# Performance work log

Hardware: AMD Instinct MI355X
Metric: run time of the kernel (lower is better)

The kernel has to match this reference:

```python
import jax, jax.numpy as jnp
import numpy as np

N_NODES = 50000
NEG_SLOPE = 0.2  # PyG GATConv default leaky_relu slope


def gat_conv(x, src, dst, W, a_src, a_dst, b, heads, out_ch, concat):
    """PyG-style GATConv. src/dst: [E] edge endpoints (messages flow src->dst)."""
    n = N_NODES
    h = (x @ W).reshape(n, heads, out_ch)            # [N, H, C]
    # per-node attention logits, gathered per edge
    s_src = (h * a_src).sum(-1)                       # [N, H]
    s_dst = (h * a_dst).sum(-1)                       # [N, H]
    e = jax.nn.leaky_relu(s_src[src] + s_dst[dst], NEG_SLOPE)  # [E, H]
    # segment softmax over incoming edges of each dst node
    e_max = jax.ops.segment_max(e, dst, num_segments=n)        # [N, H]
    ex = jnp.exp(e - e_max[dst])                                # [E, H]
    denom = jax.ops.segment_sum(ex, dst, num_segments=n)       # [N, H]
    alpha = ex / denom[dst]                                     # [E, H]
    # scatter-add weighted messages
    out = jax.ops.segment_sum(h[src] * alpha[:, :, None], dst, num_segments=n)  # [N, H, C]
    if concat:
        out = out.reshape(n, heads * out_ch)
    else:
        out = out.mean(axis=1)
    return out + b


def setup_inputs() -> dict:
    key = jax.random.key(0)
    ks = jax.random.split(key, 16)
    n, e = N_NODES, 400000
    in_ch, hidden, out_ch = 3, 64, 32
    x = jax.random.normal(ks[0], (n, in_ch), dtype=jnp.float32)
    edge_index = jax.random.randint(ks[1], (2, e), 0, n, dtype=jnp.int32)

    def glorot(k, shape):
        fan = sum(shape)
        return jax.random.uniform(k, shape, jnp.float32, -1.0, 1.0) * jnp.sqrt(6.0 / fan)

    # layer 1: in=3 -> hidden=64, heads=4, concat
    W1 = glorot(ks[2], (in_ch, 4 * hidden))
    a_src1 = glorot(ks[3], (4, hidden))
    a_dst1 = glorot(ks[4], (4, hidden))
    b1 = jnp.zeros((4 * hidden,), jnp.float32)
    # layer 2: 256 -> 64, heads=4, concat
    W2 = glorot(ks[5], (4 * hidden, 4 * hidden))
    a_src2 = glorot(ks[6], (4, hidden))
    a_dst2 = glorot(ks[7], (4, hidden))
    b2 = jnp.zeros((4 * hidden,), jnp.float32)
    # layer 3: 256 -> 32, heads=1, mean (concat=False)
    W3 = glorot(ks[8], (4 * hidden, out_ch))
    a_src3 = glorot(ks[9], (1, out_ch))
    a_dst3 = glorot(ks[10], (1, out_ch))
    b3 = jnp.zeros((out_ch,), jnp.float32)
    return dict(x=x, edge_index=edge_index,
                W1=W1, a_src1=a_src1, a_dst1=a_dst1, b1=b1,
                W2=W2, a_src2=a_src2, a_dst2=a_dst2, b2=b2,
                W3=W3, a_src3=a_src3, a_dst3=a_dst3, b3=b3)


def reference(x, edge_index,
              W1, a_src1, a_dst1, b1,
              W2, a_src2, a_dst2, b2,
              W3, a_src3, a_dst3, b3):
    n = N_NODES
    loops = jnp.arange(n, dtype=edge_index.dtype)
    src = jnp.concatenate([edge_index[0], loops])  # PyG adds self-loops by default
    dst = jnp.concatenate([edge_index[1], loops])
    h = gat_conv(x, src, dst, W1, a_src1, a_dst1, b1, heads=4, out_ch=64, concat=True)
    h = jax.nn.relu(h)  # dropout is identity in eval mode
    h = gat_conv(h, src, dst, W2, a_src2, a_dst2, b2, heads=4, out_ch=64, concat=True)
    h = jax.nn.relu(h)
    out = gat_conv(h, src, dst, W3, a_src3, a_dst3, b3, heads=1, out_ch=32, concat=False)
    return out
```

## Files before the change

kernel.cpp:

```cpp
#include <hip/hip_runtime.h>
#include <math.h>


#define NEG_SLOPE 0.2f
#define CAP 40

typedef unsigned short u16;
typedef short bf16x8 __attribute__((ext_vector_type(8)));
typedef float floatx4 __attribute__((ext_vector_type(4)));

__device__ __forceinline__ float b2f(u16 u) {
    return __uint_as_float(((unsigned int)u) << 16);
}
__device__ __forceinline__ u16 f2b(float f) {
    unsigned int u = __float_as_uint(f);
    unsigned int r = (u + 0x7fffu + ((u >> 16) & 1u)) >> 16;
    return (u16)r;
}
__device__ __forceinline__ void load16(const u16* g, u16* l) {
    __builtin_amdgcn_global_load_lds(
        (const __attribute__((address_space(1))) void*)g,
        (__attribute__((address_space(3))) void*)l, 16, 0, 0);
}


__device__ __forceinline__ void pack_dev(const float* __restrict__ W,
                                         u16* __restrict__ Bhi,
                                         u16* __restrict__ Blo, int N, int idx) {
    int CT = N / 16;
    int lane = idx & 63;
    int ctkb = idx >> 6;
    int ct = ctkb % CT;
    int kb = ctkb / CT;
    int col = ct * 16 + (lane & 15);
    int k0 = kb * 32 + (lane >> 4) * 8;
#pragma unroll
    for (int j = 0; j < 8; ++j) {
        float w = W[(size_t)(k0 + j) * N + col];
        u16 hi = f2b(w);
        Bhi[(size_t)idx * 8 + j] = hi;
        Blo[(size_t)idx * 8 + j] = f2b(w - b2f(hi));
    }
}


__global__ __launch_bounds__(256) void fill_prep(
    const int* __restrict__ ei,
    const float* __restrict__ W1, const float* __restrict__ as1,
    const float* __restrict__ ad1,
    const float* __restrict__ W2, const float* __restrict__ W3,
    u16* __restrict__ B2h, u16* __restrict__ B2l,
    u16* __restrict__ B3h, u16* __restrict__ B3l,
    float* __restrict__ vsd, int* __restrict__ cursor,
    int* __restrict__ csr, int n, int E) {
    const int tid = threadIdx.x;
    const int tg = blockIdx.x * 256 + tid;
    const int NTH = gridDim.x * 256;
    const int Etot = E + n;
    const int lane = tid & 63;

    if (tg < 8192) {
        pack_dev(W2, B2h, B2l, 256, tg);
    } else if (tg < 9216) {
        pack_dev(W3, B3h, B3l, 32, tg - 8192);
    } else if (tg < 9472) {
        int j = tg - 9216;
        float a_s = as1[j], a_d = ad1[j];
#pragma unroll
        for (int k = 0; k < 3; ++k) {
            float w = W1[k * 256 + j];
            float ps = w * a_s, pd = w * a_d;
#pragma unroll
            for (int o = 32; o > 0; o >>= 1) {
                ps += __shfl_xor(ps, o);
                pd += __shfl_xor(pd, o);
            }
            if (lane == 0) {
                vsd[(j >> 6) * 3 + k] = ps;
                vsd[12 + (j >> 6) * 3 + k] = pd;
            }
        }
    }
    for (int e = tg; e < Etot; e += NTH) {
        int src, dst;
        if (e < E) { src = ei[e]; dst = ei[E + e]; }
        else       { src = e - E; dst = e - E; }
        int old = atomicAdd(&cursor[dst], 1);
        if (old < CAP) csr[dst * CAP + old] = src;
    }
}


__global__ __launch_bounds__(256) void gat_aggregate_l1(const float* __restrict__ x,
                                                        const float* __restrict__ vsd,
                                                        const int* __restrict__ cur,
                                                        const int* __restrict__ csr,
                                                        const float* __restrict__ W1,
                                                        const float* __restrict__ bias,
                                                        u16* __restrict__ outHi,
                                                        u16* __restrict__ outLo, int n) {
    int node = blockIdx.x * 4 + (threadIdx.x >> 6);
    int lane = threadIdx.x & 63;
    if (node >= n) return;
    const int hB = lane & 3;
    const int eL = lane >> 2;
    const int hA = lane >> 4;
    int beg = node * CAP;
    int end = beg + min(cur[node], CAP);

    float vs0 = vsd[hB * 3 + 0], vs1 = vsd[hB * 3 + 1], vs2 = vsd[hB * 3 + 2];
    float vd0 = vsd[12 + hB * 3 + 0], vd1 = vsd[12 + hB * 3 + 1], vd2 = vsd[12 + hB * 3 + 2];
    float xd0 = x[node * 3 + 0], xd1 = x[node * 3 + 1], xd2 = x[node * 3 + 2];
    float sd = fmaf(xd0, vd0, fmaf(xd1, vd1, xd2 * vd2));

    float m = -INFINITY, l = 0.f;
    float ax = 0.f, ay = 0.f, az = 0.f;

    for (int base = beg; base < end; base += 16) {
        int j = base + eL;
        bool valid = (j < end);
        int sj = valid ? csr[j] : 0;
        float x0 = x[sj * 3 + 0];
        float x1 = x[sj * 3 + 1];
        float x2 = x[sj * 3 + 2];
        float logit = -INFINITY;
        if (valid) {
            float xv = fmaf(x0, vs0, fmaf(x1, vs1, x2 * vs2)) + sd;
            logit = (xv > 0.f) ? xv : NEG_SLOPE * xv;
        }
        float cm = logit;
        cm = fmaxf(cm, __shfl_xor(cm, 4));
        cm = fmaxf(cm, __shfl_xor(cm, 8));
        cm = fmaxf(cm, __shfl_xor(cm, 16));
        cm = fmaxf(cm, __shfl_xor(cm, 32));
        float nm = fmaxf(m, cm);
        float scale = __expf(m - nm);
        float ex = valid ? __expf(logit - nm) : 0.f;
        float es = ex;
        es += __shfl_xor(es, 4);
        es += __shfl_xor(es, 8);
        es += __shfl_xor(es, 16);
        es += __shfl_xor(es, 32);
        l = l * scale + es;
        m = nm;
        float sA = __shfl(scale, hA);
        ax *= sA; ay *= sA; az *= sA;

        int cnt = min(16, end - base);
        for (int t = 0; t < cnt; ++t) {
            float a  = __shfl(ex, t * 4 + hA);
            float bx = __shfl(x0, t * 4);
            float by = __shfl(x1, t * 4);
            float bz = __shfl(x2, t * 4);
            ax = fmaf(a, bx, ax);
            ay = fmaf(a, by, ay);
            az = fmaf(a, bz, az);
        }
    }

    float lf = __shfl(l, hA);
    float inv = 1.f / lf;
    ax *= inv; ay *= inv; az *= inv;

    int c = lane * 4;
    const float4 w0 = *(const float4*)&W1[0 * 256 + c];
    const float4 w1 = *(const float4*)&W1[1 * 256 + c];
    const float4 w2 = *(const float4*)&W1[2 * 256 + c];
    const float4 bv = *(const float4*)&bias[c];
    float4 o;
    o.x = fmaxf(fmaf(ax, w0.x, fmaf(ay, w1.x, fmaf(az, w2.x, bv.x))), 0.f);
    o.y = fmaxf(fmaf(ax, w0.y, fmaf(ay, w1.y, fmaf(az, w2.y, bv.y))), 0.f);
    o.z = fmaxf(fmaf(ax, w0.z, fmaf(ay, w1.z, fmaf(az, w2.z, bv.z))), 0.f);
    o.w = fmaxf(fmaf(ax, w0.w, fmaf(ay, w1.w, fmaf(az, w2.w, bv.w))), 0.f);
    ushort4 h4, l4;
    h4.x = f2b(o.x); l4.x = f2b(o.x - b2f(h4.x));
    h4.y = f2b(o.y); l4.y = f2b(o.y - b2f(h4.y));
    h4.z = f2b(o.z); l4.z = f2b(o.z - b2f(h4.z));
    h4.w = f2b(o.w); l4.w = f2b(o.w - b2f(h4.w));
    *(ushort4*)&outHi[(size_t)node * 256 + c] = h4;
    *(ushort4*)&outLo[(size_t)node * 256 + c] = l4;
}


template <int CT, int HEADS>
__global__ __launch_bounds__(512, 4) void gemm_async(const u16* __restrict__ Ahi,
                                                     const u16* __restrict__ Alo,
                                                     const u16* __restrict__ Bhi,
                                                     const u16* __restrict__ Blo,
                                                     const float* __restrict__ asrc,
                                                     const float* __restrict__ adst,
                                                     u16* __restrict__ Hb,
                                                     float* __restrict__ ssrc,
                                                     float* __restrict__ sdst, int n) {
    constexpr int THREADS = 512;
    constexpr int BFRAG = CT * 64;
    constexpr int BSZ = BFRAG * 8;
    __shared__ __align__(16) u16 lds[2][2 * BSZ];

    int t = threadIdx.x;
    int w = t >> 6, l = t & 63;
    int m0 = blockIdx.x * 128 + w * 16;
    int lm = l & 15, q = l >> 4;

    int arow = min(m0 + lm, n - 1);
    const u16* aH = Ahi + (size_t)arow * 256 + q * 8;
    const u16* aL = Alo + (size_t)arow * 256 + q * 8;

    floatx4 acc[CT] = {};

    auto stageB = [&](int buf, int kb) {
        u16* L = &lds[buf][0];
        constexpr int BROUNDS = (BFRAG + THREADS - 1) / THREADS;
#pragma unroll
        for (int r = 0; r < BROUNDS; ++r) {
            int u = r * THREADS + t;
            if ((BFRAG % THREADS == 0) || u < BFRAG) {
                size_t off = ((size_t)kb * BFRAG + (size_t)u) * 8;
                u16* Lb = L + (size_t)(r * THREADS + w * 64) * 8;
                load16(Bhi + off, Lb);
                load16(Blo + off, Lb + BSZ);
            }
        }
    };

    stageB(0, 0);
    bf16x8 ahi = *(const bf16x8*)aH;
    bf16x8 alo = *(const bf16x8*)aL;
    __syncthreads();

    for (int kb = 0; kb < 8; ++kb) {
        int cur = kb & 1;
        bf16x8 nhi = ahi, nlo = alo;
        if (kb < 7) {
            stageB(cur ^ 1, kb + 1);
            nhi = *(const bf16x8*)(aH + (kb + 1) * 32);
            nlo = *(const bf16x8*)(aL + (kb + 1) * 32);
        }
        const u16* L = &lds[cur][0];
#pragma unroll
        for (int ct = 0; ct < CT; ++ct) {
            bf16x8 bhi = *(const bf16x8*)&L[(ct * 64 + l) * 8];
            bf16x8 blo = *(const bf16x8*)&L[BSZ + (ct * 64 + l) * 8];
            acc[ct] = __builtin_amdgcn_mfma_f32_16x16x32_bf16(ahi, bhi, acc[ct], 0, 0, 0);
            acc[ct] = __builtin_amdgcn_mfma_f32_16x16x32_bf16(alo, bhi, acc[ct], 0, 0, 0);
            acc[ct] = __builtin_amdgcn_mfma_f32_16x16x32_bf16(ahi, blo, acc[ct], 0, 0, 0);
        }
        __syncthreads();
        ahi = nhi; alo = nlo;
    }

#pragma unroll
    for (int ct = 0; ct < CT; ++ct) {
#pragma unroll
        for (int r = 0; r < 4; ++r) {
            int row = m0 + q * 4 + r;
            if (row < n)
                Hb[(size_t)row * (CT * 16) + ct * 16 + lm] = f2b(acc[ct][r]);
        }
    }
    constexpr int CPH = CT / HEADS;
    float ps[4][HEADS] = {}, pd[4][HEADS] = {};
#pragma unroll
    for (int h = 0; h < HEADS; ++h) {
#pragma unroll
        for (int j = 0; j < CPH; ++j) {
            int ct = h * CPH + j;
            float a_s = asrc[ct * 16 + lm];
            float a_d = adst[ct * 16 + lm];
#pragma unroll
            for (int r = 0; r < 4; ++r) {
                ps[r][h] = fmaf(acc[ct][r], a_s, ps[r][h]);
                pd[r][h] = fmaf(acc[ct][r], a_d, pd[r][h]);
            }
        }
    }
#pragma unroll
    for (int r = 0; r < 4; ++r)
#pragma unroll
        for (int h = 0; h < HEADS; ++h)
#pragma unroll
            for (int o = 1; o < 16; o <<= 1) {
                ps[r][h] += __shfl_xor(ps[r][h], o);
                pd[r][h] += __shfl_xor(pd[r][h], o);
            }
#pragma unroll
    for (int h = 0; h < HEADS; ++h) {
        if (lm == h) {
#pragma unroll
            for (int r = 0; r < 4; ++r) {
                int row = m0 + q * 4 + r;
                if (row < n) {
                    ssrc[row * HEADS + h] = ps[r][h];
                    sdst[row * HEADS + h] = pd[r][h];
                }
            }
        }
    }
}


__global__ __launch_bounds__(256) void gat_aggregate_m4(const u16* __restrict__ Hb,
                                                        const float* __restrict__ ssrc,
                                                        const float* __restrict__ sdst,
                                                        const int* __restrict__ cur,
                                                        const int* __restrict__ csr,
                                                        const float* __restrict__ bias,
                                                        u16* __restrict__ outHi,
                                                        u16* __restrict__ outLo, int n) {
    int node = blockIdx.x * 4 + (threadIdx.x >> 6);
    int lane = threadIdx.x & 63;
    if (node >= n) return;
    const int hB = lane & 3;
    const int eL = lane >> 2;
    const int hA = lane >> 4;
    int beg = node * CAP;
    int end = beg + min(cur[node], CAP);
    float sd = sdst[node * 4 + hB];
    float m = -INFINITY, l = 0.f;
    float4 acc = make_float4(0.f, 0.f, 0.f, 0.f);

    for (int base = beg; base < end; base += 16) {
        int j = base + eL;
        bool valid = (j < end);
        int sj = valid ? csr[j] : 0;
        float logit = -INFINITY;
        if (valid) {
            float xv = ssrc[sj * 4 + hB] + sd;
            logit = (xv > 0.f) ? xv : NEG_SLOPE * xv;
        }
        float cm = logit;
        cm = fmaxf(cm, __shfl_xor(cm, 4));
        cm = fmaxf(cm, __shfl_xor(cm, 8));
        cm = fmaxf(cm, __shfl_xor(cm, 16));
        cm = fmaxf(cm, __shfl_xor(cm, 32));
        float nm = fmaxf(m, cm);
        float scale = __expf(m - nm);
        float ex = valid ? __expf(logit - nm) : 0.f;
        float es = ex;
        es += __shfl_xor(es, 4);
        es += __shfl_xor(es, 8);
        es += __shfl_xor(es, 16);
        es += __shfl_xor(es, 32);
        l = l * scale + es;
        m = nm;
        float sA = __shfl(scale, hA);
        acc.x *= sA; acc.y *= sA; acc.z *= sA; acc.w *= sA;

        int cnt = min(16, end - base);
        for (int t = 0; t < cnt; t += 4) {
#pragma unroll
            for (int u = 0; u < 4; ++u) {
                int tt = t + u;
                float a = __shfl(ex, tt * 4 + hA);
                int s = __shfl(sj, tt * 4);
                ushort4 hv = *(const ushort4*)&Hb[(size_t)s * 256 + lane * 4];
                acc.x = fmaf(a, b2f(hv.x), acc.x);
                acc.y = fmaf(a, b2f(hv.y), acc.y);
                acc.z = fmaf(a, b2f(hv.z), acc.z);
                acc.w = fmaf(a, b2f(hv.w), acc.w);
            }
        }
    }
    float lf = __shfl(l, hA);
    float inv = 1.f / lf;
    const float4 bv = *(const float4*)&bias[lane * 4];
    float4 o;
    o.x = fmaxf(fmaf(acc.x, inv, bv.x), 0.f);
    o.y = fmaxf(fmaf(acc.y, inv, bv.y), 0.f);
    o.z = fmaxf(fmaf(acc.z, inv, bv.z), 0.f);
    o.w = fmaxf(fmaf(acc.w, inv, bv.w), 0.f);
    ushort4 h4, l4;
    h4.x = f2b(o.x); l4.x = f2b(o.x - b2f(h4.x));
    h4.y = f2b(o.y); l4.y = f2b(o.y - b2f(h4.y));
    h4.z = f2b(o.z); l4.z = f2b(o.z - b2f(h4.z));
    h4.w = f2b(o.w); l4.w = f2b(o.w - b2f(h4.w));
    *(ushort4*)&outHi[(size_t)node * 256 + lane * 4] = h4;
    *(ushort4*)&outLo[(size_t)node * 256 + lane * 4] = l4;
}


__global__ __launch_bounds__(256) void gat_aggregate_h1(const u16* __restrict__ Hb,
                                                        const float* __restrict__ ssrc,
                                                        const float* __restrict__ sdst,
                                                        const int* __restrict__ cur,
                                                        const int* __restrict__ csr,
                                                        const float* __restrict__ bias,
                                                        float* __restrict__ out, int n) {
    int node = blockIdx.x * 4 + (threadIdx.x >> 6);
    int lane = threadIdx.x & 63;
    if (node >= n) return;
    int dg = min(cur[node], CAP);
    int beg = node * CAP;
    float sd = sdst[node];

    bool valid = (lane < dg);
    int sj = valid ? csr[beg + lane] : 0;
    float logit = -INFINITY;
    if (valid) {
        float xv = ssrc[sj] + sd;
        logit = (xv > 0.f) ? xv : NEG_SLOPE * xv;
    }
    float cm = logit;
#pragma unroll
    for (int o = 32; o > 0; o >>= 1) cm = fmaxf(cm, __shfl_xor(cm, o));
    float ex = valid ? __expf(logit - cm) : 0.f;
    float l = ex;
#pragma unroll
    for (int o = 32; o > 0; o >>= 1) l += __shfl_xor(l, o);

    const int eh = lane >> 5;
    const int ch = lane & 31;
    float acc = 0.f;
    for (int t = 0; t < dg; t += 8) {
#pragma unroll
        for (int u = 0; u < 4; ++u) {
            int e = t + u * 2 + eh;
            float a = __shfl(ex, e & 63);
            int s = __shfl(sj, e & 63);
            if (e < dg) acc = fmaf(a, b2f(Hb[(size_t)s * 32 + ch]), acc);
        }
    }
    acc += __shfl_xor(acc, 32);
    if (lane < 32) out[(size_t)node * 32 + lane] = acc / l + bias[lane];
}


extern "C" void kernel_launch(void* const* d_in, const int* in_sizes, int n_in,
                              void* d_out, int out_size, void* d_ws, size_t ws_size,
                              hipStream_t stream) {
    const float* x   = (const float*)d_in[0];
    const int*   ei  = (const int*)d_in[1];
    const float* W1  = (const float*)d_in[2];
    const float* as1 = (const float*)d_in[3];
    const float* ad1 = (const float*)d_in[4];
    const float* b1  = (const float*)d_in[5];
    const float* W2  = (const float*)d_in[6];
    const float* as2 = (const float*)d_in[7];
    const float* ad2 = (const float*)d_in[8];
    const float* b2  = (const float*)d_in[9];
    const float* W3  = (const float*)d_in[10];
    const float* as3 = (const float*)d_in[11];
    const float* ad3 = (const float*)d_in[12];
    const float* b3  = (const float*)d_in[13];
    float* out = (float*)d_out;

    const int n = in_sizes[0] / 3;
    const int E = in_sizes[1] / 2;
    const int Etot = E + n;

    char* ws = (char*)d_ws;
    u16* Fhi  = (u16*)ws;    ws += (size_t)n * 256 * sizeof(u16);
    u16* Flo  = (u16*)ws;    ws += (size_t)n * 256 * sizeof(u16);
    u16* Hb   = (u16*)ws;    ws += (size_t)n * 256 * sizeof(u16);
    u16* Hb3  = (u16*)ws;    ws += (size_t)n * 32 * sizeof(u16);
    u16* B2h  = (u16*)ws;    ws += (size_t)8 * 16 * 64 * 8 * sizeof(u16);
    u16* B2l  = (u16*)ws;    ws += (size_t)8 * 16 * 64 * 8 * sizeof(u16);
    u16* B3h  = (u16*)ws;    ws += (size_t)8 * 2 * 64 * 8 * sizeof(u16);
    u16* B3l  = (u16*)ws;    ws += (size_t)8 * 2 * 64 * 8 * sizeof(u16);
    float* ssrc = (float*)ws;  ws += (size_t)n * 4 * sizeof(float);
    float* sdst = (float*)ws;  ws += (size_t)n * 4 * sizeof(float);
    float* vsd  = (float*)ws;  ws += 32 * sizeof(float);
    int* cursor = (int*)ws;    ws += (size_t)n * sizeof(int);
    int* csr    = (int*)ws;    ws += (size_t)n * CAP * sizeof(int);

    hipMemsetAsync(cursor, 0, (size_t)n * sizeof(int), stream);

    int eblocks = (Etot + 255) / 256;
    int nb4 = (n + 3) / 4;
    int nb128 = (n + 127) / 128;

    fill_prep<<<eblocks, 256, 0, stream>>>(ei, W1, as1, ad1, W2, W3,
                                           B2h, B2l, B3h, B3l, vsd,
                                           cursor, csr, n, E);

    gat_aggregate_l1<<<nb4, 256, 0, stream>>>(x, vsd, cursor, csr, W1, b1,
                                              Fhi, Flo, n);

    gemm_async<16, 4><<<nb128, 512, 0, stream>>>(Fhi, Flo, B2h, B2l, as2, ad2,
                                                 Hb, ssrc, sdst, n);

    gat_aggregate_m4<<<nb4, 256, 0, stream>>>(Hb, ssrc, sdst, cursor, csr,
                                              b2, Fhi, Flo, n);

    gemm_async<2, 1><<<nb128, 512, 0, stream>>>(Fhi, Flo, B3h, B3l, as3, ad3,
                                                Hb3, ssrc, sdst, n);

    gat_aggregate_h1<<<nb4, 256, 0, stream>>>(Hb3, ssrc, sdst, cursor, csr,
                                              b3, out, n);
}
```

Before: 248.1 us.

## Fuse layer-3 linear projection and attention scores into layer-2 aggregation epilogue

The layer-2 aggregation kernel now keeps each node's 256-wide ReLU output in shared memory and computes the 32-wide layer-3 projection directly with FP32 dot products against a transposed W3, along with the source and destination attention scores. This removes the hi/lo bf16 write of the intermediate features, the separate layer-3 MFMA GEMM launch and its reread of those features. The trade-off is extra per-wave scalar FMA work and W3T reads (32KB, cache-resident) in the aggregation kernel. Separate ssrc3/sdst3 buffers are added to avoid overwriting the layer-2 scores still being read by other blocks.

```diff
diff --git a/kernel.cpp b/kernel.cpp
--- a/kernel.cpp
+++ b/kernel.cpp
@@ -50,7 +50,7 @@
     const float* __restrict__ ad1,
     const float* __restrict__ W2, const float* __restrict__ W3,
     u16* __restrict__ B2h, u16* __restrict__ B2l,
-    u16* __restrict__ B3h, u16* __restrict__ B3l,
+    float* __restrict__ W3T,
     float* __restrict__ vsd, int* __restrict__ cursor,
     int* __restrict__ csr, int n, int E) {
     const int tid = threadIdx.x;
@@ -61,10 +61,12 @@
 
     if (tg < 8192) {
         pack_dev(W2, B2h, B2l, 256, tg);
-    } else if (tg < 9216) {
-        pack_dev(W3, B3h, B3l, 32, tg - 8192);
-    } else if (tg < 9472) {
-        int j = tg - 9216;
+    } else if (tg < 16384) {
+        int idx = tg - 8192;
+        int k = idx >> 5, j = idx & 31;
+        W3T[j * 256 + k] = W3[k * 32 + j];
+    } else if (tg < 16640) {
+        int j = tg - 16384;
         float a_s = as1[j], a_d = ad1[j];
 #pragma unroll
         for (int k = 0; k < 3; ++k) {
@@ -305,9 +307,15 @@
                                                         const int* __restrict__ cur,
                                                         const int* __restrict__ csr,
                                                         const float* __restrict__ bias,
-                                                        u16* __restrict__ outHi,
-                                                        u16* __restrict__ outLo, int n) {
-    int node = blockIdx.x * 4 + (threadIdx.x >> 6);
+                                                        const float* __restrict__ W3T,
+                                                        const float* __restrict__ as3,
+                                                        const float* __restrict__ ad3,
+                                                        u16* __restrict__ Hb3,
+                                                        float* __restrict__ ssrc3,
+                                                        float* __restrict__ sdst3, int n) {
+    __shared__ float sO[4][256];
+    int wv = threadIdx.x >> 6;
+    int node = blockIdx.x * 4 + wv;
     int lane = threadIdx.x & 63;
     if (node >= n) return;
     const int hB = lane & 3;
@@ -369,13 +377,32 @@
     o.y = fmaxf(fmaf(acc.y, inv, bv.y), 0.f);
     o.z = fmaxf(fmaf(acc.z, inv, bv.z), 0.f);
     o.w = fmaxf(fmaf(acc.w, inv, bv.w), 0.f);
-    ushort4 h4, l4;
-    h4.x = f2b(o.x); l4.x = f2b(o.x - b2f(h4.x));
-    h4.y = f2b(o.y); l4.y = f2b(o.y - b2f(h4.y));
-    h4.z = f2b(o.z); l4.z = f2b(o.z - b2f(h4.z));
-    h4.w = f2b(o.w); l4.w = f2b(o.w - b2f(h4.w));
-    *(ushort4*)&outHi[(size_t)node * 256 + lane * 4] = h4;
-    *(ushort4*)&outLo[(size_t)node * 256 + lane * 4] = l4;
+
+    *(float4*)&sO[wv][lane * 4] = o;
+    const int pj = lane & 31;
+    const int kh = (lane >> 5) * 128;
+    const float* wrow = W3T + pj * 256 + kh;
+    const float* orow = &sO[wv][kh];
+    float p = 0.f;
+#pragma unroll 8
+    for (int q = 0; q < 128; q += 4) {
+        float4 ov = *(const float4*)&orow[q];
+        float4 wvv = *(const float4*)&wrow[q];
+        p = fmaf(ov.x, wvv.x, p);
+        p = fmaf(ov.y, wvv.y, p);
+        p = fmaf(ov.z, wvv.z, p);
+        p = fmaf(ov.w, wvv.w, p);
+    }
+    p += __shfl_xor(p, 32);
+    if (lane < 32) Hb3[(size_t)node * 32 + lane] = f2b(p);
+    float s_s = p * as3[pj];
+    float s_d = p * ad3[pj];
+#pragma unroll
+    for (int off = 16; off > 0; off >>= 1) {
+        s_s += __shfl_xor(s_s, off);
+        s_d += __shfl_xor(s_d, off);
+    }
+    if (lane == 0) { ssrc3[node] = s_s; sdst3[node] = s_d; }
 }
 
 
@@ -455,10 +482,11 @@
     u16* Hb3  = (u16*)ws;    ws += (size_t)n * 32 * sizeof(u16);
     u16* B2h  = (u16*)ws;    ws += (size_t)8 * 16 * 64 * 8 * sizeof(u16);
     u16* B2l  = (u16*)ws;    ws += (size_t)8 * 16 * 64 * 8 * sizeof(u16);
-    u16* B3h  = (u16*)ws;    ws += (size_t)8 * 2 * 64 * 8 * sizeof(u16);
-    u16* B3l  = (u16*)ws;    ws += (size_t)8 * 2 * 64 * 8 * sizeof(u16);
+    float* W3T = (float*)ws;   ws += (size_t)32 * 256 * sizeof(float);
     float* ssrc = (float*)ws;  ws += (size_t)n * 4 * sizeof(float);
     float* sdst = (float*)ws;  ws += (size_t)n * 4 * sizeof(float);
+    float* ssrc3 = (float*)ws; ws += (size_t)n * sizeof(float);
+    float* sdst3 = (float*)ws; ws += (size_t)n * sizeof(float);
     float* vsd  = (float*)ws;  ws += 32 * sizeof(float);
     int* cursor = (int*)ws;    ws += (size_t)n * sizeof(int);
     int* csr    = (int*)ws;    ws += (size_t)n * CAP * sizeof(int);
@@ -470,7 +498,7 @@
     int nb128 = (n + 127) / 128;
 
     fill_prep<<<eblocks, 256, 0, stream>>>(ei, W1, as1, ad1, W2, W3,
-                                           B2h, B2l, B3h, B3l, vsd,
+                                           B2h, B2l, W3T, vsd,
                                            cursor, csr, n, E);
 
     gat_aggregate_l1<<<nb4, 256, 0, stream>>>(x, vsd, cursor, csr, W1, b1,
@@ -480,11 +508,9 @@
                                                  Hb, ssrc, sdst, n);
 
     gat_aggregate_m4<<<nb4, 256, 0, stream>>>(Hb, ssrc, sdst, cursor, csr,
-                                              b2, Fhi, Flo, n);
-
-    gemm_async<2, 1><<<nb128, 512, 0, stream>>>(Fhi, Flo, B3h, B3l, as3, ad3,
-                                                Hb3, ssrc, sdst, n);
-
-    gat_aggregate_h1<<<nb4, 256, 0, stream>>>(Hb3, ssrc, sdst, cursor, csr,
+                                              b2, W3T, as3, ad3,
+                                              Hb3, ssrc3, sdst3, n);
+
+    gat_aggregate_h1<<<nb4, 256, 0, stream>>>(Hb3, ssrc3, sdst3, cursor, csr,
                                               b3, out, n);
 }
```

Result: slower. 385.9 us (+55.6%).
